# Kernel tuning notes

Hardware: AMD Instinct MI355X
Metric: run time of the kernel (lower is better)

## Reference

```python
import jax, jax.numpy as jnp
import numpy as np

P, C, NX, NY, NT = 2, 1, 128, 128, 8


def setup_inputs() -> dict:
    key = jax.random.key(0)
    k1, k2 = jax.random.split(key)
    x_5D = jax.random.normal(k1, (P, C, NX, NY, NT), dtype=jnp.float32)
    # per-pixel regularization parameter map (positive)
    lambda_reg = jax.random.uniform(k2, (P, 1, NX, NY, NT), dtype=jnp.float32) * 0.1 + 1e-3
    ten = jnp.asarray(10.0, jnp.float32)  # nn.Parameter init value 10.0
    return {"x_5D": x_5D, "lambda_reg": lambda_reg, "tau": ten, "sigma": ten,
            "theta": ten, "T": 128}


def _grad_G(u):
    # u: (P,1,Nx,Ny,Nt) -> forward finite differences with circular boundary,
    # stacked over the 3 spatial/temporal dims: (P,3,Nx,Ny,Nt)
    v = u[:, 0]
    return jnp.stack([jnp.roll(v, -1, axis=a) - v for a in (1, 2, 3)], axis=1)


def _grad_GH(q):
    # adjoint of _grad_G (negative divergence): (P,3,Nx,Ny,Nt) -> (P,1,Nx,Ny,Nt)
    out = sum(jnp.roll(q[:, d], 1, axis=d + 1) - q[:, d] for d in range(3))
    return out[:, None]


def _clip_act(q, lam):
    # pointwise projection onto [-lam, lam] ball: q * lam / max(lam, |q|)
    return q * lam / jnp.maximum(lam, jnp.abs(q))


def reference(x_5D, lambda_reg, tau, sigma, theta, T):
    dtype = x_5D.dtype
    # L = sqrt(op_norm_AHA^2 + op_norm_GHG^2) = sqrt(1 + 12)
    L = jnp.sqrt(jnp.asarray(13.0, dtype))
    sig = jax.nn.sigmoid(sigma).astype(dtype) / L
    tau_ = jax.nn.sigmoid(tau).astype(dtype) / L
    th = jax.nn.sigmoid(theta).astype(dtype)

    xnoisy = x_5D
    x0 = x_5D
    xbar = x_5D
    p = x_5D
    q = jnp.zeros((x_5D.shape[0], 3) + x_5D.shape[2:], dtype=dtype)

    def step(carry, _):
        x0, xbar, p, q = carry
        p = (p + sig * (xbar - xnoisy)) / (1.0 + sig)
        q = _clip_act(q + sig * _grad_G(xbar), lambda_reg)
        x1 = x0 - tau_ * p - tau_ * _grad_GH(q)
        # updating xbar on the final iteration is dead code in the original
        # (it only skips unused work), so a uniform scan is mathematically identical
        xbar = x1 + th * (x1 - x0)
        return (x1, xbar, p, q), None

    (x1, _, _, _), _ = jax.lax.scan(step, (x0, xbar, p, q), None, length=T)
    return x1
```

## Files before the change

kernel.cpp:

```cpp
#include <hip/hip_runtime.h>
#include <math.h>

#define NSITES (2 * 128 * 128 * 8)
#define NBLK   256
#define NSUP   32
#define TLX    16
#define TLY    24
#define NCOL   (TLX * TLY)
#define NTHR   (NCOL * 2)

union F4 { float4 v; float f[4]; };
union U4 { uint4 v; unsigned w[4]; };

__device__ __forceinline__ unsigned bf_rnd(float v) {
    const unsigned u = __float_as_uint(v);
    return (u + 0x7FFFu + ((u >> 16) & 1u)) >> 16;
}
__device__ __forceinline__ float bf_lo(unsigned p) { return __uint_as_float(p << 16); }
__device__ __forceinline__ float bf_hi(unsigned p) { return __uint_as_float(p & 0xFFFF0000u); }
__device__ __forceinline__ unsigned pk_bf2(float lo, float hi) {
    return bf_rnd(lo) | (bf_rnd(hi) << 16);
}

template <bool FIRST, bool LAST>
__global__ __launch_bounds__(NTHR, 3) void pdhg_col(
    const float* __restrict__ x,
    const float* __restrict__ lam,
    const float* __restrict__ tau_p,
    const float* __restrict__ sigma_p,
    const float* __restrict__ theta_p,
    const unsigned long long* __restrict__ inD1,
    const unsigned long long* __restrict__ inD2,
    unsigned long long* __restrict__ outD1,
    unsigned long long* __restrict__ outD2,
    float* __restrict__ out_final)
{
    __shared__ float4 Lxb[2][NTHR];
    __shared__ uint4  Lqq[2][NTHR];

    const int b  = 32 * (blockIdx.x & 7) + (blockIdx.x >> 3);
    const int pp = b >> 7;
    const int rr = b & 127;
    const int bx = rr >> 3;
    const int by = rr & 7;

    const int t   = threadIdx.x;
    const int tm  = t & 1;
    const int col = t >> 1;
    const int lx  = col / TLY;
    const int ly  = col - lx * TLY;

    const int X  = ((bx << 3) + lx - 4) & 127;
    const int Y  = ((by << 4) + ly - 4) & 127;
    const int Xm = (X + 127) & 127;
    const int Ym = (Y + 127) & 127;

    const int gcol = (pp << 17) | (X << 10) | (Y << 3);
    const int gxm  = (pp << 17) | (Xm << 10) | (Y << 3);
    const int gym  = (pp << 17) | (X << 10) | (Ym << 3);

    const bool comp = (lx >= 1) && (lx < 15) && (ly >= 1) && (ly < 23);

    const float L = 3.605551275463989f;
    const float s_sig = (1.f / (1.f + __expf(-sigma_p[0]))) / L;
    const float s_tau = (1.f / (1.f + __expf(-tau_p[0]))) / L;
    const float s_th  =  1.f / (1.f + __expf(-theta_p[0]));
    const float inv1s = 1.f / (1.f + s_sig);

    const int c4 = (gcol >> 2) + tm;

    float xn[4], lamc[4], lamx[4], lamy[4];
    {
        const float4* x4 = (const float4*)x;
        const float4* l4 = (const float4*)lam;
        if (FIRST || comp) {
            F4 a; a.v = x4[c4];
            #pragma unroll
            for (int j = 0; j < 4; ++j) xn[j] = a.f[j];
        } else {
            #pragma unroll
            for (int j = 0; j < 4; ++j) xn[j] = 0.f;
        }
        if (comp) {
            F4 a;
            a.v = l4[c4];
            #pragma unroll
            for (int j = 0; j < 4; ++j) lamc[j] = a.f[j];
            a.v = l4[(gxm >> 2) + tm];
            #pragma unroll
            for (int j = 0; j < 4; ++j) lamx[j] = a.f[j];
            a.v = l4[(gym >> 2) + tm];
            #pragma unroll
            for (int j = 0; j < 4; ++j) lamy[j] = a.f[j];
        } else {
            #pragma unroll
            for (int j = 0; j < 4; ++j) { lamc[j] = 0.f; lamx[j] = 0.f; lamy[j] = 0.f; }
        }
    }
    const float lamtm = __shfl_xor(lamc[3], 1, 64);

    float x0[4], p[4], q0[4], q1[4], q2[4], xb[4];
    if (FIRST) {
        #pragma unroll
        for (int j = 0; j < 4; ++j) {
            const float v = xn[j];
            x0[j] = v; p[j] = v; xb[j] = v;
            q0[j] = 0.f; q1[j] = 0.f; q2[j] = 0.f;
        }
    } else {
        const uint4* d1 = (const uint4*)inD1;
        const int base = (gcol >> 1) + 2 * tm;
        #pragma unroll
        for (int k = 0; k < 2; ++k) {
            U4 a; a.v = d1[base + k];
            #pragma unroll
            for (int m = 0; m < 2; ++m) {
                const int j = 2 * k + m;
                const unsigned lo = a.w[2 * m], hi = a.w[2 * m + 1];
                xb[j] = bf_lo(lo); q0[j] = bf_hi(lo);
                q1[j] = bf_lo(hi); q2[j] = bf_hi(hi);
            }
        }
        if (comp) {
            const float4* d2 = (const float4*)inD2;
            #pragma unroll
            for (int k = 0; k < 2; ++k) {
                F4 a; a.v = d2[base + k];
                p[2 * k]     = a.f[0]; x0[2 * k]     = a.f[1];
                p[2 * k + 1] = a.f[2]; x0[2 * k + 1] = a.f[3];
            }
        } else {
            #pragma unroll
            for (int j = 0; j < 4; ++j) { p[j] = 0.f; x0[j] = 0.f; }
        }
    }

    auto clip = [](float v, float l) { return fmaxf(-l, fminf(l, v)); };

    auto substep = [&](const int h) {
        const int pb = h & 1;
        if (lx >= 3 - h && lx < 13 + h && ly >= 3 - h && ly < 21 + h) {
            Lxb[pb][t] = make_float4(xb[0], xb[1], xb[2], xb[3]);
            U4 w;
            w.w[0] = pk_bf2(q0[0], q1[0]); w.w[1] = pk_bf2(q0[1], q1[1]);
            w.w[2] = pk_bf2(q0[2], q1[2]); w.w[3] = pk_bf2(q0[3], q1[3]);
            Lqq[pb][t] = w.v;
        }
        __syncthreads();
        if (lx >= 4 - h && lx < 12 + h && ly >= 4 - h && ly < 20 + h) {
            const float xb_tp = __shfl_xor(xb[0], 1, 64);
            const float xb_tm = __shfl_xor(xb[3], 1, 64);
            const float q2_tm = __shfl_xor(q2[3], 1, 64);
            F4 xp, xm, yp, ym; U4 qx, qy;
            xp.v = Lxb[pb][t + 2 * TLY];
            xm.v = Lxb[pb][t - 2 * TLY];
            yp.v = Lxb[pb][t + 2];
            ym.v = Lxb[pb][t - 2];
            qx.v = Lqq[pb][t - 2 * TLY];
            qy.v = Lqq[pb][t - 2];
            float oxb[4], oq2[4];
            #pragma unroll
            for (int j = 0; j < 4; ++j) { oxb[j] = xb[j]; oq2[j] = q2[j]; }
            #pragma unroll
            for (int j = 0; j < 4; ++j) {
                const float ob   = oxb[j];
                const float xbtp = (j < 3) ? oxb[j + 1] : xb_tp;
                const float xbtm = (j > 0) ? oxb[j - 1] : xb_tm;
                const float q2tm = (j > 0) ? oq2[j - 1] : q2_tm;
                const float lT   = (j > 0) ? lamc[j - 1] : lamtm;
                const float pn  = (p[j] + s_sig * (ob - xn[j])) * inv1s;
                const float q0n = clip(q0[j] + s_sig * (xp.f[j] - ob), lamc[j]);
                const float q1n = clip(q1[j] + s_sig * (yp.f[j] - ob), lamc[j]);
                const float q2n = clip(oq2[j] + s_sig * (xbtp - ob), lamc[j]);
                const float q0m = clip(bf_lo(qx.w[j]) + s_sig * (ob - xm.f[j]), lamx[j]);
                const float q1m = clip(bf_hi(qy.w[j]) + s_sig * (ob - ym.f[j]), lamy[j]);
                const float q2m = clip(q2tm + s_sig * (ob - xbtm), lT);
                const float dv  = (q0m - q0n) + (q1m - q1n) + (q2m - q2n);
                const float x1  = x0[j] - s_tau * (pn + dv);
                xb[j] = x1 + s_th * (x1 - x0[j]);
                x0[j] = x1; p[j] = pn;
                q0[j] = q0n; q1[j] = q1n; q2[j] = q2n;
            }
        }
    };

    substep(3);
    substep(2);
    substep(1);
    substep(0);

    if (lx >= 4 && lx < 12 && ly >= 4 && ly < 20) {
        if (LAST) {
            float4* o4 = (float4*)out_final;
            F4 a;
            a.f[0] = x0[0]; a.f[1] = x0[1]; a.f[2] = x0[2]; a.f[3] = x0[3];
            o4[c4] = a.v;
        } else {
            uint4*  o1 = (uint4*)outD1;
            float4* o2 = (float4*)outD2;
            const int base = (gcol >> 1) + 2 * tm;
            #pragma unroll
            for (int k = 0; k < 2; ++k) {
                U4 w;
                #pragma unroll
                for (int m = 0; m < 2; ++m) {
                    const int j = 2 * k + m;
                    w.w[2 * m]     = pk_bf2(xb[j], q0[j]);
                    w.w[2 * m + 1] = pk_bf2(q1[j], q2[j]);
                }
                o1[base + k] = w.v;
                F4 d;
                d.f[0] = p[2 * k];     d.f[1] = x0[2 * k];
                d.f[2] = p[2 * k + 1]; d.f[3] = x0[2 * k + 1];
                o2[base + k] = d.v;
            }
        }
    }
}

extern "C" void kernel_launch(void* const* d_in, const int* in_sizes, int n_in,
                              void* d_out, int out_size, void* d_ws, size_t ws_size,
                              hipStream_t stream) {
    const float* x   = (const float*)d_in[0];
    const float* lam = (const float*)d_in[1];
    const float* tau = (const float*)d_in[2];
    const float* sig = (const float*)d_in[3];
    const float* th  = (const float*)d_in[4];
    float* out = (float*)d_out;

    unsigned long long* D1 = (unsigned long long*)d_ws;
    unsigned long long* D2 = D1 + 2 * (size_t)NSITES;

    dim3 grid(NBLK), block(NTHR);

    for (int g = 0; g < NSUP; ++g) {
        const size_t si = (size_t)((g + 1) & 1) * NSITES;
        const size_t so = (size_t)(g & 1) * NSITES;
        const unsigned long long *i1 = D1 + si, *i2 = D2 + si;
        unsigned long long *o1 = D1 + so, *o2 = D2 + so;
        if (g == 0) {
            pdhg_col<true, false><<<grid, block, 0, stream>>>(
                x, lam, tau, sig, th, i1, i2, o1, o2, out);
        } else if (g == NSUP - 1) {
            pdhg_col<false, true><<<grid, block, 0, stream>>>(
                x, lam, tau, sig, th, i1, i2, o1, o2, out);
        } else {
            pdhg_col<false, false><<<grid, block, 0, stream>>>(
                x, lam, tau, sig, th, i1, i2, o1, o2, out);
        }
    }
}
```

Measured before the change: 285.2 us.

## Fuse 32 temporal-blocked launches into one persistent cooperative kernel with grid barrier

New measurement: 1.110 ms. 289% more time.

```diff
diff --git a/kernel.cpp b/kernel.cpp
--- a/kernel.cpp
+++ b/kernel.cpp
@@ -4,11 +4,14 @@
 #define NSITES (2 * 128 * 128 * 8)
 #define NBLK   256
 #define NSUP   32
+#define NSYNC  (NSUP - 1)
 #define TLX    16
 #define TLY    24
 #define NCOL   (TLX * TLY)
 #define NTHR   (NCOL * 2)
 
+__device__ unsigned g_bar = 0;
+
 union F4 { float4 v; float f[4]; };
 union U4 { uint4 v; unsigned w[4]; };
 
@@ -21,18 +24,18 @@
 __device__ __forceinline__ unsigned pk_bf2(float lo, float hi) {
     return bf_rnd(lo) | (bf_rnd(hi) << 16);
 }
-
-template <bool FIRST, bool LAST>
-__global__ __launch_bounds__(NTHR, 3) void pdhg_col(
+__device__ __forceinline__ float bf_round(float v) {
+    return __uint_as_float(bf_rnd(v) << 16);
+}
+
+__global__ __launch_bounds__(NTHR, 3) void pdhg_persist(
     const float* __restrict__ x,
     const float* __restrict__ lam,
     const float* __restrict__ tau_p,
     const float* __restrict__ sigma_p,
     const float* __restrict__ theta_p,
-    const unsigned long long* __restrict__ inD1,
-    const unsigned long long* __restrict__ inD2,
-    unsigned long long* __restrict__ outD1,
-    unsigned long long* __restrict__ outD2,
+    unsigned long long* __restrict__ D1g,
+    unsigned long long* __restrict__ D2g,
     float* __restrict__ out_final)
 {
     __shared__ float4 Lxb[2][NTHR];
@@ -60,6 +63,13 @@
     const int gym  = (pp << 17) | (X << 10) | (Ym << 3);
 
     const bool comp = (lx >= 1) && (lx < 15) && (ly >= 1) && (ly < 23);
+    const bool own  = (lx >= 4) && (lx < 12) && (ly >= 4) && (ly < 20);
+
+    unsigned bar_base = 0;
+    if (t == 0) {
+        const unsigned v = atomicAdd(&g_bar, 0u);
+        bar_base = (v / (unsigned)(NSYNC * NBLK)) * (unsigned)(NSYNC * NBLK);
+    }
 
     const float L = 3.605551275463989f;
     const float s_sig = (1.f / (1.f + __expf(-sigma_p[0]))) / L;
@@ -73,66 +83,28 @@
     {
         const float4* x4 = (const float4*)x;
         const float4* l4 = (const float4*)lam;
-        if (FIRST || comp) {
-            F4 a; a.v = x4[c4];
-            #pragma unroll
-            for (int j = 0; j < 4; ++j) xn[j] = a.f[j];
-        } else {
-            #pragma unroll
-            for (int j = 0; j < 4; ++j) xn[j] = 0.f;
-        }
-        if (comp) {
-            F4 a;
-            a.v = l4[c4];
-            #pragma unroll
-            for (int j = 0; j < 4; ++j) lamc[j] = a.f[j];
-            a.v = l4[(gxm >> 2) + tm];
-            #pragma unroll
-            for (int j = 0; j < 4; ++j) lamx[j] = a.f[j];
-            a.v = l4[(gym >> 2) + tm];
-            #pragma unroll
-            for (int j = 0; j < 4; ++j) lamy[j] = a.f[j];
-        } else {
-            #pragma unroll
-            for (int j = 0; j < 4; ++j) { lamc[j] = 0.f; lamx[j] = 0.f; lamy[j] = 0.f; }
-        }
+        F4 a;
+        a.v = x4[c4];
+        #pragma unroll
+        for (int j = 0; j < 4; ++j) xn[j] = a.f[j];
+        a.v = l4[c4];
+        #pragma unroll
+        for (int j = 0; j < 4; ++j) lamc[j] = a.f[j];
+        a.v = l4[(gxm >> 2) + tm];
+        #pragma unroll
+        for (int j = 0; j < 4; ++j) lamx[j] = a.f[j];
+        a.v = l4[(gym >> 2) + tm];
+        #pragma unroll
+        for (int j = 0; j < 4; ++j) lamy[j] = a.f[j];
     }
     const float lamtm = __shfl_xor(lamc[3], 1, 64);
 
     float x0[4], p[4], q0[4], q1[4], q2[4], xb[4];
-    if (FIRST) {
-        #pragma unroll
-        for (int j = 0; j < 4; ++j) {
-            const float v = xn[j];
-            x0[j] = v; p[j] = v; xb[j] = v;
-            q0[j] = 0.f; q1[j] = 0.f; q2[j] = 0.f;
-        }
-    } else {
-        const uint4* d1 = (const uint4*)inD1;
-        const int base = (gcol >> 1) + 2 * tm;
-        #pragma unroll
-        for (int k = 0; k < 2; ++k) {
-            U4 a; a.v = d1[base + k];
-            #pragma unroll
-            for (int m = 0; m < 2; ++m) {
-                const int j = 2 * k + m;
-                const unsigned lo = a.w[2 * m], hi = a.w[2 * m + 1];
-                xb[j] = bf_lo(lo); q0[j] = bf_hi(lo);
-                q1[j] = bf_lo(hi); q2[j] = bf_hi(hi);
-            }
-        }
-        if (comp) {
-            const float4* d2 = (const float4*)inD2;
-            #pragma unroll
-            for (int k = 0; k < 2; ++k) {
-                F4 a; a.v = d2[base + k];
-                p[2 * k]     = a.f[0]; x0[2 * k]     = a.f[1];
-                p[2 * k + 1] = a.f[2]; x0[2 * k + 1] = a.f[3];
-            }
-        } else {
-            #pragma unroll
-            for (int j = 0; j < 4; ++j) { p[j] = 0.f; x0[j] = 0.f; }
-        }
+    #pragma unroll
+    for (int j = 0; j < 4; ++j) {
+        const float v = xn[j];
+        x0[j] = v; p[j] = v; xb[j] = v;
+        q0[j] = 0.f; q1[j] = 0.f; q2[j] = 0.f;
     }
 
     auto clip = [](float v, float l) { return fmaxf(-l, fminf(l, v)); };
@@ -184,37 +156,88 @@
         }
     };
 
-    substep(3);
-    substep(2);
-    substep(1);
-    substep(0);
-
-    if (lx >= 4 && lx < 12 && ly >= 4 && ly < 20) {
-        if (LAST) {
-            float4* o4 = (float4*)out_final;
-            F4 a;
-            a.f[0] = x0[0]; a.f[1] = x0[1]; a.f[2] = x0[2]; a.f[3] = x0[3];
-            o4[c4] = a.v;
-        } else {
-            uint4*  o1 = (uint4*)outD1;
-            float4* o2 = (float4*)outD2;
-            const int base = (gcol >> 1) + 2 * tm;
-            #pragma unroll
-            for (int k = 0; k < 2; ++k) {
-                U4 w;
+    #pragma unroll 1
+    for (int g = 0; g < NSUP; ++g) {
+        if (g > 0) {
+            if (own) {
                 #pragma unroll
-                for (int m = 0; m < 2; ++m) {
-                    const int j = 2 * k + m;
-                    w.w[2 * m]     = pk_bf2(xb[j], q0[j]);
-                    w.w[2 * m + 1] = pk_bf2(q1[j], q2[j]);
-                }
-                o1[base + k] = w.v;
-                F4 d;
-                d.f[0] = p[2 * k];     d.f[1] = x0[2 * k];
-                d.f[2] = p[2 * k + 1]; d.f[3] = x0[2 * k + 1];
-                o2[base + k] = d.v;
-            }
-        }
+                for (int j = 0; j < 4; ++j) {
+                    xb[j] = bf_round(xb[j]);
+                    q0[j] = bf_round(q0[j]);
+                    q1[j] = bf_round(q1[j]);
+                    q2[j] = bf_round(q2[j]);
+                }
+            } else {
+                const size_t si = (size_t)((g & 1) ^ 1) * NSITES;
+                const uint4* d1 = (const uint4*)(D1g + si);
+                const int base = (gcol >> 1) + 2 * tm;
+                #pragma unroll
+                for (int k = 0; k < 2; ++k) {
+                    U4 a; a.v = d1[base + k];
+                    #pragma unroll
+                    for (int m = 0; m < 2; ++m) {
+                        const int j = 2 * k + m;
+                        const unsigned lo = a.w[2 * m], hi = a.w[2 * m + 1];
+                        xb[j] = bf_lo(lo); q0[j] = bf_hi(lo);
+                        q1[j] = bf_lo(hi); q2[j] = bf_hi(hi);
+                    }
+                }
+                if (comp) {
+                    const float4* d2 = (const float4*)(D2g + si);
+                    #pragma unroll
+                    for (int k = 0; k < 2; ++k) {
+                        F4 a; a.v = d2[base + k];
+                        p[2 * k]     = a.f[0]; x0[2 * k]     = a.f[1];
+                        p[2 * k + 1] = a.f[2]; x0[2 * k + 1] = a.f[3];
+                    }
+                }
+            }
+        }
+
+        substep(3);
+        substep(2);
+        substep(1);
+        substep(0);
+
+        if (g < NSUP - 1) {
+            if (own) {
+                const size_t so = (size_t)(g & 1) * NSITES;
+                uint4*  o1 = (uint4*)(D1g + so);
+                float4* o2 = (float4*)(D2g + so);
+                const int base = (gcol >> 1) + 2 * tm;
+                #pragma unroll
+                for (int k = 0; k < 2; ++k) {
+                    U4 w;
+                    #pragma unroll
+                    for (int m = 0; m < 2; ++m) {
+                        const int j = 2 * k + m;
+                        w.w[2 * m]     = pk_bf2(xb[j], q0[j]);
+                        w.w[2 * m + 1] = pk_bf2(q1[j], q2[j]);
+                    }
+                    o1[base + k] = w.v;
+                    F4 d;
+                    d.f[0] = p[2 * k];     d.f[1] = x0[2 * k];
+                    d.f[2] = p[2 * k + 1]; d.f[3] = x0[2 * k + 1];
+                    o2[base + k] = d.v;
+                }
+            }
+            __syncthreads();
+            if (t == 0) {
+                __threadfence();
+                atomicAdd(&g_bar, 1u);
+                const unsigned want = bar_base + (unsigned)((g + 1) * NBLK);
+                while (atomicAdd(&g_bar, 0u) < want) __builtin_amdgcn_s_sleep(8);
+                __threadfence();
+            }
+            __syncthreads();
+        }
+    }
+
+    if (own) {
+        float4* o4 = (float4*)out_final;
+        F4 a;
+        a.f[0] = x0[0]; a.f[1] = x0[1]; a.f[2] = x0[2]; a.f[3] = x0[3];
+        o4[c4] = a.v;
     }
 }
 
@@ -231,22 +254,8 @@
     unsigned long long* D1 = (unsigned long long*)d_ws;
     unsigned long long* D2 = D1 + 2 * (size_t)NSITES;
 
-    dim3 grid(NBLK), block(NTHR);
-
-    for (int g = 0; g < NSUP; ++g) {
-        const size_t si = (size_t)((g + 1) & 1) * NSITES;
-        const size_t so = (size_t)(g & 1) * NSITES;
-        const unsigned long long *i1 = D1 + si, *i2 = D2 + si;
-        unsigned long long *o1 = D1 + so, *o2 = D2 + so;
-        if (g == 0) {
-            pdhg_col<true, false><<<grid, block, 0, stream>>>(
-                x, lam, tau, sig, th, i1, i2, o1, o2, out);
-        } else if (g == NSUP - 1) {
-            pdhg_col<false, true><<<grid, block, 0, stream>>>(
-                x, lam, tau, sig, th, i1, i2, o1, o2, out);
-        } else {
-            pdhg_col<false, false><<<grid, block, 0, stream>>>(
-                x, lam, tau, sig, th, i1, i2, o1, o2, out);
-        }
-    }
-}
+    void* args[] = { (void*)&x, (void*)&lam, (void*)&tau, (void*)&sig, (void*)&th,
+                     (void*)&D1, (void*)&D2, (void*)&out };
+    hipLaunchCooperativeKernel(pdhg_persist, dim3(NBLK), dim3(NTHR),
+                               args, 0, stream);
+}
```
